# Kernel optimization log

Hardware: AMD Instinct MI355X
Metric: run time of the kernel (lower is better)

The kernel has to match this reference:

```python
import jax, jax.numpy as jnp
import numpy as np

N_NODES = 50000
N_EDGES = 800000
IN_DIM_NODE = 128
IN_DIM_EDGE = 16
OUT_DIM = 32
N_HEAD = 4


def setup_inputs() -> dict:
    key = jax.random.key(0)
    ks = jax.random.split(key, 8)
    feats_node = jax.random.normal(ks[0], (N_NODES, IN_DIM_NODE), dtype=jnp.float32)
    feats_edge = jax.random.normal(ks[1], (N_EDGES, IN_DIM_EDGE), dtype=jnp.float32)
    src = jax.random.randint(ks[2], (N_EDGES,), 0, N_NODES)
    dst = jax.random.randint(ks[3], (N_EDGES,), 0, N_NODES)
    # params: init normal(std=0.5) as in the torch module
    W_node = 0.5 * jax.random.normal(ks[4], (N_HEAD * OUT_DIM, IN_DIM_NODE), dtype=jnp.float32)
    attn_l = 0.5 * jax.random.normal(ks[5], (N_HEAD, OUT_DIM), dtype=jnp.float32)
    attn_r = 0.5 * jax.random.normal(ks[6], (N_HEAD, OUT_DIM), dtype=jnp.float32)
    attn_e = 0.5 * jax.random.normal(ks[7], (N_HEAD, IN_DIM_EDGE), dtype=jnp.float32)
    return {"feats_node": feats_node, "feats_edge": feats_edge, "src": src,
            "dst": dst, "W_node": W_node, "attn_l": attn_l, "attn_r": attn_r,
            "attn_e": attn_e}


def reference(feats_node, feats_edge, src, dst, W_node, attn_l, attn_r, attn_e):
    N = feats_node.shape[0]
    H, D = attn_l.shape
    # node projection: [N, H, D]
    feat_n = (feats_node @ W_node.T).reshape(N, H, D)
    # per-node attention logits: [N, H]
    el = jnp.einsum('nhd,hd->nh', feat_n, attn_l)
    er = jnp.einsum('nhd,hd->nh', feat_n, attn_r)
    # per-edge (edge-feature) logit: [E, H]
    ee = jnp.einsum('ef,hf->eh', feats_edge, attn_e)
    # gather logits along edges and apply leaky relu (slope 0.2)
    e = jax.nn.leaky_relu(el[src] + er[dst] + ee, negative_slope=0.2)  # [E, H]
    # edge softmax segmented by destination node (numerically stable)
    m = jax.ops.segment_max(e, dst, num_segments=N)          # [N, H]
    m = jnp.where(jnp.isfinite(m), m, 0.0)                   # guard 0-degree nodes
    e_exp = jnp.exp(e - m[dst])                               # [E, H]
    s = jax.ops.segment_sum(e_exp, dst, num_segments=N)       # [N, H]
    a = e_exp / s[dst]                                        # [E, H]
    # weighted scatter-aggregate: sum over in-edges of a * ft[src]
    msg = feat_n[src] * a[:, :, None]                          # [E, H, D]
    out = jax.ops.segment_sum(msg, dst, num_segments=N)       # [N, H, D]
    return out.reshape(N, H * D)
```

## Files before the change

kernel.cpp:

```cpp
#include <hip/hip_runtime.h>
#include <hip/hip_bf16.h>
#include <math.h>

#define NN 50000
#define NE 800000
#define SCAN_NB ((NN + 255) / 256)
#define PROJ_ROWS_PER_BLOCK 112
#define PROJ_NBLK ((NN + PROJ_ROWS_PER_BLOCK - 1) / PROJ_ROWS_PER_BLOCK)

__global__ __launch_bounds__(256) void k_proj2(
    const float* __restrict__ X, const float* __restrict__ W,
    const float* __restrict__ al, const float* __restrict__ ar,
    __hip_bfloat16* __restrict__ FB, float* __restrict__ el, float* __restrict__ er)
{
    extern __shared__ char smem[];
    float* WtW = (float*)smem;
    float* Xs  = (float*)(smem + 64 * 64 * 8);

    const int t = threadIdx.x;
    const int wave = t >> 6, lane = t & 63;

    const float alv0 = al[lane], alv1 = al[lane + 64];
    const float arv0 = ar[lane], arv1 = ar[lane + 64];
    const int rowBase = blockIdx.x * PROJ_ROWS_PER_BLOCK;
    const float2* WtP = (const float2*)WtW;

    for (int g = 0; g < 7; ++g) {
        int r0 = rowBase + g * 16;
        __syncthreads();
#pragma unroll
        for (int i = 0; i < 2; ++i) {
            int idx = t + i * 256;
            int rr = idx >> 5, c4 = (idx & 31) * 4;
            int r = r0 + rr;
            float4 v = make_float4(0.f, 0.f, 0.f, 0.f);
            if (r < NN) v = *reinterpret_cast<const float4*>(X + (size_t)r * 128 + c4);
            *reinterpret_cast<float4*>(&Xs[rr * 128 + c4]) = v;
        }

        float a00 = 0.f, a01 = 0.f, a10 = 0.f, a11 = 0.f;
        float a20 = 0.f, a21 = 0.f, a30 = 0.f, a31 = 0.f;

        for (int kc = 0; kc < 2; ++kc) {
            if (kc) __syncthreads();
#pragma unroll
            for (int it = 0; it < 8; ++it) {
                int flat = t + it * 256;
                int c = flat & 127, q = flat >> 7;
                float4 v = *reinterpret_cast<const float4*>(
                    W + (size_t)c * 128 + kc * 64 + q * 4);
                int base = (c & 63) * 2 + (c >> 6);
                WtW[(q * 4 + 0) * 128 + base] = v.x;
                WtW[(q * 4 + 1) * 128 + base] = v.y;
                WtW[(q * 4 + 2) * 128 + base] = v.z;
                WtW[(q * 4 + 3) * 128 + base] = v.w;
            }
            __syncthreads();

            const float* xr0 = &Xs[(wave * 4 + 0) * 128 + kc * 64];
            const float* xr1 = &Xs[(wave * 4 + 1) * 128 + kc * 64];
            const float* xr2 = &Xs[(wave * 4 + 2) * 128 + kc * 64];
            const float* xr3 = &Xs[(wave * 4 + 3) * 128 + kc * 64];
#pragma unroll 2
            for (int k4 = 0; k4 < 16; ++k4) {
                float2 wa = WtP[(k4 * 4 + 0) * 64 + lane];
                float2 wb = WtP[(k4 * 4 + 1) * 64 + lane];
                float2 wc = WtP[(k4 * 4 + 2) * 64 + lane];
                float2 wd = WtP[(k4 * 4 + 3) * 64 + lane];
                float4 x0 = *reinterpret_cast<const float4*>(&xr0[k4 * 4]);
                float4 x1 = *reinterpret_cast<const float4*>(&xr1[k4 * 4]);
                float4 x2 = *reinterpret_cast<const float4*>(&xr2[k4 * 4]);
                float4 x3 = *reinterpret_cast<const float4*>(&xr3[k4 * 4]);
                a00 += x0.x * wa.x + x0.y * wb.x + x0.z * wc.x + x0.w * wd.x;
                a01 += x0.x * wa.y + x0.y * wb.y + x0.z * wc.y + x0.w * wd.y;
                a10 += x1.x * wa.x + x1.y * wb.x + x1.z * wc.x + x1.w * wd.x;
                a11 += x1.x * wa.y + x1.y * wb.y + x1.z * wc.y + x1.w * wd.y;
                a20 += x2.x * wa.x + x2.y * wb.x + x2.z * wc.x + x2.w * wd.x;
                a21 += x2.x * wa.y + x2.y * wb.y + x2.z * wc.y + x2.w * wd.y;
                a30 += x3.x * wa.x + x3.y * wb.x + x3.z * wc.x + x3.w * wd.x;
                a31 += x3.x * wa.y + x3.y * wb.y + x3.z * wc.y + x3.w * wd.y;
            }
        }

        float ar0[4] = {a00, a10, a20, a30};
        float ar1[4] = {a01, a11, a21, a31};
#pragma unroll
        for (int r = 0; r < 4; ++r) {
            int row = r0 + wave * 4 + r;
            if (row < NN) {
                FB[(size_t)row * 128 + lane]      = __float2bfloat16(ar0[r]);
                FB[(size_t)row * 128 + lane + 64] = __float2bfloat16(ar1[r]);
                float pl = ar0[r] * alv0, pr = ar0[r] * arv0;
                float ql = ar1[r] * alv1, qr = ar1[r] * arv1;
#pragma unroll
                for (int off = 16; off; off >>= 1) {
                    pl += __shfl_xor(pl, off);
                    pr += __shfl_xor(pr, off);
                    ql += __shfl_xor(ql, off);
                    qr += __shfl_xor(qr, off);
                }
                if ((lane & 31) == 0) {
                    int h = lane >> 5;
                    el[row * 4 + h]     = pl;
                    er[row * 4 + h]     = pr;
                    el[row * 4 + 2 + h] = ql;
                    er[row * 4 + 2 + h] = qr;
                }
            }
        }
    }
}

__global__ void k_edge_logits(const float* __restrict__ FE, const int* __restrict__ src,
                              const int* __restrict__ dst, const float* __restrict__ ae,
                              const float* __restrict__ el, const float* __restrict__ er,
                              float* __restrict__ logits, int* __restrict__ count) {
    int e = blockIdx.x * blockDim.x + threadIdx.x;
    if (e >= NE) return;
    float fe[16];
#pragma unroll
    for (int i = 0; i < 4; ++i) {
        float4 v = *reinterpret_cast<const float4*>(FE + (size_t)e * 16 + i * 4);
        fe[i * 4 + 0] = v.x; fe[i * 4 + 1] = v.y; fe[i * 4 + 2] = v.z; fe[i * 4 + 3] = v.w;
    }
    int s = src[e], d = dst[e];
    float4 elv = *reinterpret_cast<const float4*>(el + (size_t)s * 4);
    float4 erv = *reinterpret_cast<const float4*>(er + (size_t)d * 4);
    float base[4] = {elv.x, elv.y, elv.z, elv.w};
    float basr[4] = {erv.x, erv.y, erv.z, erv.w};
    float o[4];
#pragma unroll
    for (int h = 0; h < 4; ++h) {
        float ee = 0.f;
#pragma unroll
        for (int i = 0; i < 16; ++i) ee += fe[i] * ae[h * 16 + i];
        float v = base[h] + basr[h] + ee;
        o[h] = v > 0.f ? v : 0.2f * v;
    }
    *reinterpret_cast<float4*>(logits + (size_t)e * 4) = make_float4(o[0], o[1], o[2], o[3]);
    atomicAdd(&count[d], 1);
}

__global__ __launch_bounds__(256) void k_scan_a(const int* __restrict__ count,
                                                int* __restrict__ pre,
                                                int* __restrict__ bsum) {
    __shared__ int buf[256];
    int t = threadIdx.x;
    int gid = blockIdx.x * 256 + t;
    int v = (gid < NN) ? count[gid] : 0;
    int x = v;
    buf[t] = x;
    __syncthreads();
    for (int off = 1; off < 256; off <<= 1) {
        int add = (t >= off) ? buf[t - off] : 0;
        __syncthreads();
        x += add;
        buf[t] = x;
        __syncthreads();
    }
    if (gid < NN) pre[gid] = x - v;
    if (t == 255) bsum[blockIdx.x] = x;
}

__global__ __launch_bounds__(256) void k_scan_b(const int* __restrict__ bsum,
                                                int* __restrict__ bofs) {
    __shared__ int buf[256];
    int t = threadIdx.x;
    int v = (t < SCAN_NB) ? bsum[t] : 0;
    int x = v;
    buf[t] = x;
    __syncthreads();
    for (int off = 1; off < 256; off <<= 1) {
        int add = (t >= off) ? buf[t - off] : 0;
        __syncthreads();
        x += add;
        buf[t] = x;
        __syncthreads();
    }
    if (t < SCAN_NB) bofs[t] = x - v;
    if (t == 255) bofs[SCAN_NB] = x;
}

__global__ __launch_bounds__(256) void k_scan_c(int* __restrict__ pre,
                                                const int* __restrict__ bofs,
                                                int* __restrict__ cursor) {
    int gid = blockIdx.x * 256 + threadIdx.x;
    if (gid < NN) {
        int val = pre[gid] + bofs[gid >> 8];
        pre[gid] = val;
        cursor[gid] = val;
    }
    if (gid == 0) pre[NN] = bofs[SCAN_NB];
}

__global__ void k_fill(const int* __restrict__ dst, int* __restrict__ cursor,
                       int* __restrict__ edge_list) {
    int e = blockIdx.x * blockDim.x + threadIdx.x;
    if (e >= NE) return;
    int d = dst[e];
    int pos = atomicAdd(&cursor[d], 1);
    edge_list[pos] = e;
}

__global__ __launch_bounds__(256) void k_aggr2(const __hip_bfloat16* __restrict__ FB,
                                               const int* __restrict__ src,
                                               const float* __restrict__ logits,
                                               const int* __restrict__ row_ptr,
                                               const int* __restrict__ edge_list,
                                               float* __restrict__ out) {
    int wid = threadIdx.x >> 6;
    int lane = threadIdx.x & 63;
    int node = blockIdx.x * 4 + wid;
    if (node >= NN) return;
    int s0 = row_ptr[node], s1 = row_ptr[node + 1];
    float2* o2 = reinterpret_cast<float2*>(out + (size_t)node * 128);
    if (s1 == s0) { o2[lane] = make_float2(0.f, 0.f); return; }

    float m0 = -1e30f, m1 = -1e30f, m2 = -1e30f, m3 = -1e30f;
    for (int i = s0 + lane; i < s1; i += 64) {
        int e = edge_list[i];
        float4 lg = *reinterpret_cast<const float4*>(logits + (size_t)e * 4);
        m0 = fmaxf(m0, lg.x); m1 = fmaxf(m1, lg.y);
        m2 = fmaxf(m2, lg.z); m3 = fmaxf(m3, lg.w);
    }
#pragma unroll
    for (int off = 32; off; off >>= 1) {
        m0 = fmaxf(m0, __shfl_xor(m0, off));
        m1 = fmaxf(m1, __shfl_xor(m1, off));
        m2 = fmaxf(m2, __shfl_xor(m2, off));
        m3 = fmaxf(m3, __shfl_xor(m3, off));
    }
    float s0f = 0.f, s1f = 0.f, s2f = 0.f, s3f = 0.f;
    for (int i = s0 + lane; i < s1; i += 64) {
        int e = edge_list[i];
        float4 lg = *reinterpret_cast<const float4*>(logits + (size_t)e * 4);
        s0f += __expf(lg.x - m0); s1f += __expf(lg.y - m1);
        s2f += __expf(lg.z - m2); s3f += __expf(lg.w - m3);
    }
#pragma unroll
    for (int off = 32; off; off >>= 1) {
        s0f += __shfl_xor(s0f, off);
        s1f += __shfl_xor(s1f, off);
        s2f += __shfl_xor(s2f, off);
        s3f += __shfl_xor(s3f, off);
    }

    int ha = lane >> 4;
    float mh = (ha == 0) ? m0 : (ha == 1) ? m1 : (ha == 2) ? m2 : m3;
    float sh = (ha == 0) ? s0f : (ha == 1) ? s1f : (ha == 2) ? s2f : s3f;
    float rh = 1.f / sh;
    const unsigned short* FBu = reinterpret_cast<const unsigned short*>(FB);
    float acc0 = 0.f, acc1 = 0.f;
    int i = s0;
    for (; i + 1 < s1; i += 2) {
        int e0 = edge_list[i], e1 = edge_list[i + 1];
        int v0 = src[e0], v1 = src[e1];
        float lg0 = logits[(size_t)e0 * 4 + ha];
        float lg1 = logits[(size_t)e1 * 4 + ha];
        ushort2 f0 = *reinterpret_cast<const ushort2*>(FBu + (size_t)v0 * 128 + 2 * lane);
        ushort2 f1 = *reinterpret_cast<const ushort2*>(FBu + (size_t)v1 * 128 + 2 * lane);
        float w0 = __expf(lg0 - mh) * rh;
        float w1 = __expf(lg1 - mh) * rh;
        acc0 += w0 * __uint_as_float((unsigned)f0.x << 16)
              + w1 * __uint_as_float((unsigned)f1.x << 16);
        acc1 += w0 * __uint_as_float((unsigned)f0.y << 16)
              + w1 * __uint_as_float((unsigned)f1.y << 16);
    }
    if (i < s1) {
        int e0 = edge_list[i];
        int v0 = src[e0];
        float lg0 = logits[(size_t)e0 * 4 + ha];
        ushort2 f0 = *reinterpret_cast<const ushort2*>(FBu + (size_t)v0 * 128 + 2 * lane);
        float w0 = __expf(lg0 - mh) * rh;
        acc0 += w0 * __uint_as_float((unsigned)f0.x << 16);
        acc1 += w0 * __uint_as_float((unsigned)f0.y << 16);
    }
    o2[lane] = make_float2(acc0, acc1);
}

extern "C" void kernel_launch(void* const* d_in, const int* in_sizes, int n_in,
                              void* d_out, int out_size, void* d_ws, size_t ws_size,
                              hipStream_t stream) {
    const float* feats_node = (const float*)d_in[0];
    const float* feats_edge = (const float*)d_in[1];
    const int*   src        = (const int*)d_in[2];
    const int*   dst        = (const int*)d_in[3];
    const float* W          = (const float*)d_in[4];
    const float* al         = (const float*)d_in[5];
    const float* ar         = (const float*)d_in[6];
    const float* ae         = (const float*)d_in[7];
    float* out = (float*)d_out;

    char* ws = (char*)d_ws;
    size_t off = 0;
    __hip_bfloat16* feat_b = (__hip_bfloat16*)(ws + off); off += (size_t)NN * 128 * 2;
    float* el     = (float*)(ws + off); off += (size_t)NN * 4 * 4;
    float* er     = (float*)(ws + off); off += (size_t)NN * 4 * 4;
    float* logits = (float*)(ws + off); off += (size_t)NE * 4 * 4;
    int* count    = (int*)(ws + off);   off += (size_t)NN * 4;
    int* row_ptr  = (int*)(ws + off);   off += (size_t)(NN + 16) * 4;
    int* cursor   = (int*)(ws + off);   off += (size_t)NN * 4;
    int* bsum     = (int*)(ws + off);   off += (size_t)(SCAN_NB + 16) * 4;
    int* bofs     = (int*)(ws + off);   off += (size_t)(SCAN_NB + 16) * 4;
    int* edge_list= (int*)(ws + off);   off += (size_t)NE * 4;

    hipMemsetAsync(count, 0, (size_t)NN * 4, stream);

    size_t proj_lds = 64 * 64 * 8 + 16 * 128 * 4;
    k_proj2<<<PROJ_NBLK, 256, proj_lds, stream>>>(feats_node, W, al, ar, feat_b, el, er);
    k_edge_logits<<<(NE + 255) / 256, 256, 0, stream>>>(feats_edge, src, dst, ae, el, er,
                                                        logits, count);
    k_scan_a<<<SCAN_NB, 256, 0, stream>>>(count, row_ptr, bsum);
    k_scan_b<<<1, 256, 0, stream>>>(bsum, bofs);
    k_scan_c<<<SCAN_NB, 256, 0, stream>>>(row_ptr, bofs, cursor);
    k_fill<<<(NE + 255) / 256, 256, 0, stream>>>(dst, cursor, edge_list);
    k_aggr2<<<(NN + 3) / 4, 256, 0, stream>>>(feat_b, src, logits, row_ptr, edge_list, out);
}
```

Before: 361.1 us.

## Scatter logits and src into CSR order, register-resident projection, wider aggregation

A lightweight histogram kernel now runs first, and edge-logit computation is fused with the CSR fill. Each edge's logits and source index are written directly into destination-sorted arrays, so the aggregation reads them contiguously instead of chasing edge_list indirections. The projection kernel is rewritten to keep W slices in registers across a persistent loop over rows. The aggregation now loads 16-byte bf16 chunks and processes 4 edges in parallel per wave, reducing partial sums with shuffles. The trade-offs are higher register pressure in the projection, a second pass over dst for the histogram, and more scattered writes during the fill.

```diff
diff --git a/kernel.cpp b/kernel.cpp
--- a/kernel.cpp
+++ b/kernel.cpp
@@ -5,140 +5,12 @@
 #define NN 50000
 #define NE 800000
 #define SCAN_NB ((NN + 255) / 256)
-#define PROJ_ROWS_PER_BLOCK 112
-#define PROJ_NBLK ((NN + PROJ_ROWS_PER_BLOCK - 1) / PROJ_ROWS_PER_BLOCK)
-
-__global__ __launch_bounds__(256) void k_proj2(
-    const float* __restrict__ X, const float* __restrict__ W,
-    const float* __restrict__ al, const float* __restrict__ ar,
-    __hip_bfloat16* __restrict__ FB, float* __restrict__ el, float* __restrict__ er)
-{
-    extern __shared__ char smem[];
-    float* WtW = (float*)smem;
-    float* Xs  = (float*)(smem + 64 * 64 * 8);
-
-    const int t = threadIdx.x;
-    const int wave = t >> 6, lane = t & 63;
-
-    const float alv0 = al[lane], alv1 = al[lane + 64];
-    const float arv0 = ar[lane], arv1 = ar[lane + 64];
-    const int rowBase = blockIdx.x * PROJ_ROWS_PER_BLOCK;
-    const float2* WtP = (const float2*)WtW;
-
-    for (int g = 0; g < 7; ++g) {
-        int r0 = rowBase + g * 16;
-        __syncthreads();
-#pragma unroll
-        for (int i = 0; i < 2; ++i) {
-            int idx = t + i * 256;
-            int rr = idx >> 5, c4 = (idx & 31) * 4;
-            int r = r0 + rr;
-            float4 v = make_float4(0.f, 0.f, 0.f, 0.f);
-            if (r < NN) v = *reinterpret_cast<const float4*>(X + (size_t)r * 128 + c4);
-            *reinterpret_cast<float4*>(&Xs[rr * 128 + c4]) = v;
-        }
-
-        float a00 = 0.f, a01 = 0.f, a10 = 0.f, a11 = 0.f;
-        float a20 = 0.f, a21 = 0.f, a30 = 0.f, a31 = 0.f;
-
-        for (int kc = 0; kc < 2; ++kc) {
-            if (kc) __syncthreads();
-#pragma unroll
-            for (int it = 0; it < 8; ++it) {
-                int flat = t + it * 256;
-                int c = flat & 127, q = flat >> 7;
-                float4 v = *reinterpret_cast<const float4*>(
-                    W + (size_t)c * 128 + kc * 64 + q * 4);
-                int base = (c & 63) * 2 + (c >> 6);
-                WtW[(q * 4 + 0) * 128 + base] = v.x;
-                WtW[(q * 4 + 1) * 128 + base] = v.y;
-                WtW[(q * 4 + 2) * 128 + base] = v.z;
-                WtW[(q * 4 + 3) * 128 + base] = v.w;
-            }
-            __syncthreads();
-
-            const float* xr0 = &Xs[(wave * 4 + 0) * 128 + kc * 64];
-            const float* xr1 = &Xs[(wave * 4 + 1) * 128 + kc * 64];
-            const float* xr2 = &Xs[(wave * 4 + 2) * 128 + kc * 64];
-            const float* xr3 = &Xs[(wave * 4 + 3) * 128 + kc * 64];
-#pragma unroll 2
-            for (int k4 = 0; k4 < 16; ++k4) {
-                float2 wa = WtP[(k4 * 4 + 0) * 64 + lane];
-                float2 wb = WtP[(k4 * 4 + 1) * 64 + lane];
-                float2 wc = WtP[(k4 * 4 + 2) * 64 + lane];
-                float2 wd = WtP[(k4 * 4 + 3) * 64 + lane];
-                float4 x0 = *reinterpret_cast<const float4*>(&xr0[k4 * 4]);
-                float4 x1 = *reinterpret_cast<const float4*>(&xr1[k4 * 4]);
-                float4 x2 = *reinterpret_cast<const float4*>(&xr2[k4 * 4]);
-                float4 x3 = *reinterpret_cast<const float4*>(&xr3[k4 * 4]);
-                a00 += x0.x * wa.x + x0.y * wb.x + x0.z * wc.x + x0.w * wd.x;
-                a01 += x0.x * wa.y + x0.y * wb.y + x0.z * wc.y + x0.w * wd.y;
-                a10 += x1.x * wa.x + x1.y * wb.x + x1.z * wc.x + x1.w * wd.x;
-                a11 += x1.x * wa.y + x1.y * wb.y + x1.z * wc.y + x1.w * wd.y;
-                a20 += x2.x * wa.x + x2.y * wb.x + x2.z * wc.x + x2.w * wd.x;
-                a21 += x2.x * wa.y + x2.y * wb.y + x2.z * wc.y + x2.w * wd.y;
-                a30 += x3.x * wa.x + x3.y * wb.x + x3.z * wc.x + x3.w * wd.x;
-                a31 += x3.x * wa.y + x3.y * wb.y + x3.z * wc.y + x3.w * wd.y;
-            }
-        }
-
-        float ar0[4] = {a00, a10, a20, a30};
-        float ar1[4] = {a01, a11, a21, a31};
-#pragma unroll
-        for (int r = 0; r < 4; ++r) {
-            int row = r0 + wave * 4 + r;
-            if (row < NN) {
-                FB[(size_t)row * 128 + lane]      = __float2bfloat16(ar0[r]);
-                FB[(size_t)row * 128 + lane + 64] = __float2bfloat16(ar1[r]);
-                float pl = ar0[r] * alv0, pr = ar0[r] * arv0;
-                float ql = ar1[r] * alv1, qr = ar1[r] * arv1;
-#pragma unroll
-                for (int off = 16; off; off >>= 1) {
-                    pl += __shfl_xor(pl, off);
-                    pr += __shfl_xor(pr, off);
-                    ql += __shfl_xor(ql, off);
-                    qr += __shfl_xor(qr, off);
-                }
-                if ((lane & 31) == 0) {
-                    int h = lane >> 5;
-                    el[row * 4 + h]     = pl;
-                    er[row * 4 + h]     = pr;
-                    el[row * 4 + 2 + h] = ql;
-                    er[row * 4 + 2 + h] = qr;
-                }
-            }
-        }
-    }
-}
-
-__global__ void k_edge_logits(const float* __restrict__ FE, const int* __restrict__ src,
-                              const int* __restrict__ dst, const float* __restrict__ ae,
-                              const float* __restrict__ el, const float* __restrict__ er,
-                              float* __restrict__ logits, int* __restrict__ count) {
-    int e = blockIdx.x * blockDim.x + threadIdx.x;
-    if (e >= NE) return;
-    float fe[16];
-#pragma unroll
-    for (int i = 0; i < 4; ++i) {
-        float4 v = *reinterpret_cast<const float4*>(FE + (size_t)e * 16 + i * 4);
-        fe[i * 4 + 0] = v.x; fe[i * 4 + 1] = v.y; fe[i * 4 + 2] = v.z; fe[i * 4 + 3] = v.w;
-    }
-    int s = src[e], d = dst[e];
-    float4 elv = *reinterpret_cast<const float4*>(el + (size_t)s * 4);
-    float4 erv = *reinterpret_cast<const float4*>(er + (size_t)d * 4);
-    float base[4] = {elv.x, elv.y, elv.z, elv.w};
-    float basr[4] = {erv.x, erv.y, erv.z, erv.w};
-    float o[4];
-#pragma unroll
-    for (int h = 0; h < 4; ++h) {
-        float ee = 0.f;
-#pragma unroll
-        for (int i = 0; i < 16; ++i) ee += fe[i] * ae[h * 16 + i];
-        float v = base[h] + basr[h] + ee;
-        o[h] = v > 0.f ? v : 0.2f * v;
-    }
-    *reinterpret_cast<float4*>(logits + (size_t)e * 4) = make_float4(o[0], o[1], o[2], o[3]);
-    atomicAdd(&count[d], 1);
+#define PROJ_NBLK 512
+#define PROJ_RPB ((NN + PROJ_NBLK - 1) / PROJ_NBLK)
+
+__global__ void k_hist(const int* __restrict__ dst, int* __restrict__ count) {
+    int e = blockIdx.x * 256 + threadIdx.x;
+    if (e < NE) atomicAdd(&count[dst[e]], 1);
 }
 
 __global__ __launch_bounds__(256) void k_scan_a(const int* __restrict__ count,
@@ -193,89 +65,176 @@
     if (gid == 0) pre[NN] = bofs[SCAN_NB];
 }
 
-__global__ void k_fill(const int* __restrict__ dst, int* __restrict__ cursor,
-                       int* __restrict__ edge_list) {
-    int e = blockIdx.x * blockDim.x + threadIdx.x;
+__global__ __launch_bounds__(256) void k_proj3(
+    const float* __restrict__ X, const float* __restrict__ W,
+    const float* __restrict__ al, const float* __restrict__ ar,
+    __hip_bfloat16* __restrict__ FB, float* __restrict__ el, float* __restrict__ er)
+{
+    __shared__ float Xs[16 * 128];
+    const int t = threadIdx.x;
+    const int w = t >> 6, l = t & 63;
+    const int c = w * 32 + (l & 31);
+    const int kh = (l >> 5) * 64;
+
+    float4 wreg[16];
+#pragma unroll
+    for (int j = 0; j < 16; ++j)
+        wreg[j] = *reinterpret_cast<const float4*>(W + (size_t)c * 128 + kh + j * 4);
+
+    const float alv = al[c], arv = ar[c];
+    const int rowLo = blockIdx.x * PROJ_RPB;
+    const int rowHi = (rowLo + PROJ_RPB < NN) ? rowLo + PROJ_RPB : NN;
+
+    for (int r0 = rowLo; r0 < rowHi; r0 += 16) {
+        __syncthreads();
+#pragma unroll
+        for (int i = 0; i < 2; ++i) {
+            int idx = t + i * 256;
+            int rr = idx >> 5, c4 = (idx & 31) * 4;
+            int r = r0 + rr;
+            float4 v = make_float4(0.f, 0.f, 0.f, 0.f);
+            if (r < NN) v = *reinterpret_cast<const float4*>(X + (size_t)r * 128 + c4);
+            *reinterpret_cast<float4*>(&Xs[rr * 128 + c4]) = v;
+        }
+        __syncthreads();
+        int nr = rowHi - r0; if (nr > 16) nr = 16;
+        for (int rr = 0; rr < nr; ++rr) {
+            const float4* xp = reinterpret_cast<const float4*>(&Xs[rr * 128 + kh]);
+            float a0 = 0.f, a1 = 0.f, a2 = 0.f, a3 = 0.f;
+#pragma unroll
+            for (int j = 0; j < 16; ++j) {
+                float4 x = xp[j];
+                a0 += x.x * wreg[j].x; a1 += x.y * wreg[j].y;
+                a2 += x.z * wreg[j].z; a3 += x.w * wreg[j].w;
+            }
+            float tot = (a0 + a1) + (a2 + a3);
+            tot += __shfl_xor(tot, 32);
+            int row = r0 + rr;
+            if (l < 32) FB[(size_t)row * 128 + c] = __float2bfloat16(tot);
+            float pl = tot * alv, pr = tot * arv;
+#pragma unroll
+            for (int off = 16; off; off >>= 1) {
+                pl += __shfl_xor(pl, off);
+                pr += __shfl_xor(pr, off);
+            }
+            if (l == 0) { el[row * 4 + w] = pl; er[row * 4 + w] = pr; }
+        }
+    }
+}
+
+__global__ void k_logits_fill(const float* __restrict__ FE, const int* __restrict__ src,
+                              const int* __restrict__ dst, const float* __restrict__ ae,
+                              const float* __restrict__ el, const float* __restrict__ er,
+                              int* __restrict__ cursor, float4* __restrict__ lsort,
+                              int* __restrict__ ssort) {
+    int e = blockIdx.x * 256 + threadIdx.x;
     if (e >= NE) return;
-    int d = dst[e];
+    float fe[16];
+#pragma unroll
+    for (int i = 0; i < 4; ++i) {
+        float4 v = *reinterpret_cast<const float4*>(FE + (size_t)e * 16 + i * 4);
+        fe[i * 4 + 0] = v.x; fe[i * 4 + 1] = v.y; fe[i * 4 + 2] = v.z; fe[i * 4 + 3] = v.w;
+    }
+    int s = src[e], d = dst[e];
+    float4 elv = *reinterpret_cast<const float4*>(el + (size_t)s * 4);
+    float4 erv = *reinterpret_cast<const float4*>(er + (size_t)d * 4);
+    float base[4] = {elv.x + erv.x, elv.y + erv.y, elv.z + erv.z, elv.w + erv.w};
+    float o[4];
+#pragma unroll
+    for (int h = 0; h < 4; ++h) {
+        float ee = 0.f;
+#pragma unroll
+        for (int i = 0; i < 16; ++i) ee += fe[i] * ae[h * 16 + i];
+        float v = base[h] + ee;
+        o[h] = v > 0.f ? v : 0.2f * v;
+    }
     int pos = atomicAdd(&cursor[d], 1);
-    edge_list[pos] = e;
-}
-
-__global__ __launch_bounds__(256) void k_aggr2(const __hip_bfloat16* __restrict__ FB,
-                                               const int* __restrict__ src,
-                                               const float* __restrict__ logits,
-                                               const int* __restrict__ row_ptr,
-                                               const int* __restrict__ edge_list,
-                                               float* __restrict__ out) {
-    int wid = threadIdx.x >> 6;
-    int lane = threadIdx.x & 63;
+    lsort[pos] = make_float4(o[0], o[1], o[2], o[3]);
+    ssort[pos] = s;
+}
+
+__global__ __launch_bounds__(256) void k_aggr3(
+    const __hip_bfloat16* __restrict__ FB, const float* __restrict__ lsf,
+    const int* __restrict__ ssort, const int* __restrict__ row_ptr,
+    float* __restrict__ out)
+{
+    int wid = threadIdx.x >> 6, lane = threadIdx.x & 63;
     int node = blockIdx.x * 4 + wid;
     if (node >= NN) return;
     int s0 = row_ptr[node], s1 = row_ptr[node + 1];
-    float2* o2 = reinterpret_cast<float2*>(out + (size_t)node * 128);
-    if (s1 == s0) { o2[lane] = make_float2(0.f, 0.f); return; }
-
-    float m0 = -1e30f, m1 = -1e30f, m2 = -1e30f, m3 = -1e30f;
-    for (int i = s0 + lane; i < s1; i += 64) {
-        int e = edge_list[i];
-        float4 lg = *reinterpret_cast<const float4*>(logits + (size_t)e * 4);
+    int q = lane & 15, p = lane >> 4;
+    float4* o4 = reinterpret_cast<float4*>(out + (size_t)node * 128);
+    if (s1 == s0) {
+        if (p == 0) {
+            o4[2 * q]     = make_float4(0.f, 0.f, 0.f, 0.f);
+            o4[2 * q + 1] = make_float4(0.f, 0.f, 0.f, 0.f);
+        }
+        return;
+    }
+    const float4* lsort = reinterpret_cast<const float4*>(lsf);
+
+    bool have = (s0 + lane) < s1;
+    float4 my = have ? lsort[s0 + lane] : make_float4(-1e30f, -1e30f, -1e30f, -1e30f);
+    float m0 = my.x, m1 = my.y, m2 = my.z, m3 = my.w;
+    for (int i = s0 + lane + 64; i < s1; i += 64) {
+        float4 lg = lsort[i];
         m0 = fmaxf(m0, lg.x); m1 = fmaxf(m1, lg.y);
         m2 = fmaxf(m2, lg.z); m3 = fmaxf(m3, lg.w);
     }
 #pragma unroll
     for (int off = 32; off; off >>= 1) {
-        m0 = fmaxf(m0, __shfl_xor(m0, off));
-        m1 = fmaxf(m1, __shfl_xor(m1, off));
-        m2 = fmaxf(m2, __shfl_xor(m2, off));
-        m3 = fmaxf(m3, __shfl_xor(m3, off));
-    }
-    float s0f = 0.f, s1f = 0.f, s2f = 0.f, s3f = 0.f;
-    for (int i = s0 + lane; i < s1; i += 64) {
-        int e = edge_list[i];
-        float4 lg = *reinterpret_cast<const float4*>(logits + (size_t)e * 4);
-        s0f += __expf(lg.x - m0); s1f += __expf(lg.y - m1);
-        s2f += __expf(lg.z - m2); s3f += __expf(lg.w - m3);
+        m0 = fmaxf(m0, __shfl_xor(m0, off)); m1 = fmaxf(m1, __shfl_xor(m1, off));
+        m2 = fmaxf(m2, __shfl_xor(m2, off)); m3 = fmaxf(m3, __shfl_xor(m3, off));
+    }
+    float t0 = have ? __expf(my.x - m0) : 0.f;
+    float t1 = have ? __expf(my.y - m1) : 0.f;
+    float t2 = have ? __expf(my.z - m2) : 0.f;
+    float t3 = have ? __expf(my.w - m3) : 0.f;
+    for (int i = s0 + lane + 64; i < s1; i += 64) {
+        float4 lg = lsort[i];
+        t0 += __expf(lg.x - m0); t1 += __expf(lg.y - m1);
+        t2 += __expf(lg.z - m2); t3 += __expf(lg.w - m3);
     }
 #pragma unroll
     for (int off = 32; off; off >>= 1) {
-        s0f += __shfl_xor(s0f, off);
-        s1f += __shfl_xor(s1f, off);
-        s2f += __shfl_xor(s2f, off);
-        s3f += __shfl_xor(s3f, off);
-    }
-
-    int ha = lane >> 4;
+        t0 += __shfl_xor(t0, off); t1 += __shfl_xor(t1, off);
+        t2 += __shfl_xor(t2, off); t3 += __shfl_xor(t3, off);
+    }
+
+    int ha = q >> 2;
     float mh = (ha == 0) ? m0 : (ha == 1) ? m1 : (ha == 2) ? m2 : m3;
-    float sh = (ha == 0) ? s0f : (ha == 1) ? s1f : (ha == 2) ? s2f : s3f;
+    float sh = (ha == 0) ? t0 : (ha == 1) ? t1 : (ha == 2) ? t2 : t3;
     float rh = 1.f / sh;
     const unsigned short* FBu = reinterpret_cast<const unsigned short*>(FB);
-    float acc0 = 0.f, acc1 = 0.f;
-    int i = s0;
-    for (; i + 1 < s1; i += 2) {
-        int e0 = edge_list[i], e1 = edge_list[i + 1];
-        int v0 = src[e0], v1 = src[e1];
-        float lg0 = logits[(size_t)e0 * 4 + ha];
-        float lg1 = logits[(size_t)e1 * 4 + ha];
-        ushort2 f0 = *reinterpret_cast<const ushort2*>(FBu + (size_t)v0 * 128 + 2 * lane);
-        ushort2 f1 = *reinterpret_cast<const ushort2*>(FBu + (size_t)v1 * 128 + 2 * lane);
-        float w0 = __expf(lg0 - mh) * rh;
-        float w1 = __expf(lg1 - mh) * rh;
-        acc0 += w0 * __uint_as_float((unsigned)f0.x << 16)
-              + w1 * __uint_as_float((unsigned)f1.x << 16);
-        acc1 += w0 * __uint_as_float((unsigned)f0.y << 16)
-              + w1 * __uint_as_float((unsigned)f1.y << 16);
-    }
-    if (i < s1) {
-        int e0 = edge_list[i];
-        int v0 = src[e0];
-        float lg0 = logits[(size_t)e0 * 4 + ha];
-        ushort2 f0 = *reinterpret_cast<const ushort2*>(FBu + (size_t)v0 * 128 + 2 * lane);
-        float w0 = __expf(lg0 - mh) * rh;
-        acc0 += w0 * __uint_as_float((unsigned)f0.x << 16);
-        acc1 += w0 * __uint_as_float((unsigned)f0.y << 16);
-    }
-    o2[lane] = make_float2(acc0, acc1);
+    float c0 = 0.f, c1 = 0.f, c2 = 0.f, c3 = 0.f, c4 = 0.f, c5 = 0.f, c6 = 0.f, c7 = 0.f;
+    for (int it = s0; it < s1; it += 4) {
+        int i = it + p;
+        if (i < s1) {
+            int sv = ssort[i];
+            float lg = lsf[(size_t)i * 4 + ha];
+            float wgt = __expf(lg - mh) * rh;
+            uint4 f = *reinterpret_cast<const uint4*>(FBu + (size_t)sv * 128 + q * 8);
+            c0 += wgt * __uint_as_float(f.x << 16);
+            c1 += wgt * __uint_as_float(f.x & 0xffff0000u);
+            c2 += wgt * __uint_as_float(f.y << 16);
+            c3 += wgt * __uint_as_float(f.y & 0xffff0000u);
+            c4 += wgt * __uint_as_float(f.z << 16);
+            c5 += wgt * __uint_as_float(f.z & 0xffff0000u);
+            c6 += wgt * __uint_as_float(f.w << 16);
+            c7 += wgt * __uint_as_float(f.w & 0xffff0000u);
+        }
+    }
+#pragma unroll
+    for (int off = 16; off <= 32; off <<= 1) {
+        c0 += __shfl_xor(c0, off); c1 += __shfl_xor(c1, off);
+        c2 += __shfl_xor(c2, off); c3 += __shfl_xor(c3, off);
+        c4 += __shfl_xor(c4, off); c5 += __shfl_xor(c5, off);
+        c6 += __shfl_xor(c6, off); c7 += __shfl_xor(c7, off);
+    }
+    if (p == 0) {
+        o4[2 * q]     = make_float4(c0, c1, c2, c3);
+        o4[2 * q + 1] = make_float4(c4, c5, c6, c7);
+    }
 }
 
 extern "C" void kernel_launch(void* const* d_in, const int* in_sizes, int n_in,
@@ -296,23 +255,22 @@
     __hip_bfloat16* feat_b = (__hip_bfloat16*)(ws + off); off += (size_t)NN * 128 * 2;
     float* el     = (float*)(ws + off); off += (size_t)NN * 4 * 4;
     float* er     = (float*)(ws + off); off += (size_t)NN * 4 * 4;
-    float* logits = (float*)(ws + off); off += (size_t)NE * 4 * 4;
+    float* lsort  = (float*)(ws + off); off += (size_t)NE * 4 * 4;
+    int* ssort    = (int*)(ws + off);   off += (size_t)NE * 4;
     int* count    = (int*)(ws + off);   off += (size_t)NN * 4;
     int* row_ptr  = (int*)(ws + off);   off += (size_t)(NN + 16) * 4;
     int* cursor   = (int*)(ws + off);   off += (size_t)NN * 4;
     int* bsum     = (int*)(ws + off);   off += (size_t)(SCAN_NB + 16) * 4;
     int* bofs     = (int*)(ws + off);   off += (size_t)(SCAN_NB + 16) * 4;
-    int* edge_list= (int*)(ws + off);   off += (size_t)NE * 4;
 
     hipMemsetAsync(count, 0, (size_t)NN * 4, stream);
 
-    size_t proj_lds = 64 * 64 * 8 + 16 * 128 * 4;
-    k_proj2<<<PROJ_NBLK, 256, proj_lds, stream>>>(feats_node, W, al, ar, feat_b, el, er);
-    k_edge_logits<<<(NE + 255) / 256, 256, 0, stream>>>(feats_edge, src, dst, ae, el, er,
-                                                        logits, count);
+    k_hist<<<(NE + 255) / 256, 256, 0, stream>>>(dst, count);
     k_scan_a<<<SCAN_NB, 256, 0, stream>>>(count, row_ptr, bsum);
     k_scan_b<<<1, 256, 0, stream>>>(bsum, bofs);
     k_scan_c<<<SCAN_NB, 256, 0, stream>>>(row_ptr, bofs, cursor);
-    k_fill<<<(NE + 255) / 256, 256, 0, stream>>>(dst, cursor, edge_list);
-    k_aggr2<<<(NN + 3) / 4, 256, 0, stream>>>(feat_b, src, logits, row_ptr, edge_list, out);
-}
+    k_proj3<<<PROJ_NBLK, 256, 0, stream>>>(feats_node, W, al, ar, feat_b, el, er);
+    k_logits_fill<<<(NE + 255) / 256, 256, 0, stream>>>(feats_edge, src, dst, ae, el, er,
+                                                        cursor, (float4*)lsort, ssort);
+    k_aggr3<<<(NN + 3) / 4, 256, 0, stream>>>(feat_b, lsort, ssort, row_ptr, out);
+}
```

New measurement: 323.5 us. 10.4% less time.
